# Kernel optimization log

Hardware: AMD Instinct MI355X
Metric: run time of the kernel (lower is better)

Reference implementation:

```python
import math
import jax, jax.numpy as jnp
import numpy as np

BS, N, D, H = 4, 512, 1024, 16
HD = D // H


def setup_inputs() -> dict:
    key = jax.random.key(0)
    ks = jax.random.split(key, 12)
    s = 1.0 / math.sqrt(D)
    return {
        "x": jax.random.normal(ks[0], (BS, N, D), jnp.float32),
        "r": jax.random.normal(ks[1], (BS, 3, N, N), jnp.float32),
        "bias": jax.random.normal(ks[2], (BS, H, N, N), jnp.float32),
        "mask": jax.random.randint(ks[3], (BS, 1, N, N), 0, 2, jnp.int32),
        "wq": jax.random.normal(ks[4], (D, D), jnp.float32) * s,
        "bq": jnp.zeros((D,), jnp.float32),
        "wk": jax.random.normal(ks[5], (D, D), jnp.float32) * s,
        "bk": jnp.zeros((D,), jnp.float32),
        "wv": jax.random.normal(ks[6], (D, D), jnp.float32) * s,
        "bv": jnp.zeros((D,), jnp.float32),
        "wo": jax.random.normal(ks[7], (D, 1), jnp.float32) * s,
        "bo": jnp.zeros((1,), jnp.float32),
    }


def reference(x, r, bias, mask, wq, bq, wk, bk, wv, bv, wo, bo):
    bs, n, d = x.shape
    # projections -> (bs, h, n, hd)
    q = (x @ wq + bq).reshape(bs, n, H, HD).transpose(0, 2, 1, 3)
    k = (x @ wk + bk).reshape(bs, n, H, HD).transpose(0, 2, 1, 3)
    v = (x @ wv + bv).reshape(bs, n, H, HD).transpose(0, 2, 1, 3)
    logits = jnp.einsum("bhid,bhjd->bhij", q, k) / math.sqrt(HD) + bias
    logits = jnp.where(mask == 0, jnp.float32(-1e9), logits)
    w = jax.nn.softmax(logits, axis=-1)  # (bs,h,n,n)
    # o[b,i,c,h,d] = sum_j r[b,c,i,j] * w[b,h,i,j] * v[b,h,j,d]
    o = jnp.einsum("bcij,bhij,bhjd->bichd", r, w, v)
    o = o.reshape(bs, n, 3, d)
    force = o @ wo + bo  # (bs, n, 3, 1)
    return force
```

## Files before the change

kernel.cpp:

```cpp
#include <hip/hip_runtime.h>
#include <stdint.h>

#define BSZ 4
#define NSEQ 512
#define DMOD 1024
#define NH 16
#define HD 64

typedef __attribute__((ext_vector_type(8))) short bf16x8;
typedef __attribute__((ext_vector_type(4))) float f32x4;

__device__ __forceinline__ unsigned short f2bf(float f) {
    union { float f; uint32_t u; } v; v.f = f;
    uint32_t u = v.u;
    u += 0x7FFFu + ((u >> 16) & 1u);
    return (unsigned short)(u >> 16);
}

__device__ __forceinline__ void gload_lds16(const unsigned short* g, unsigned short* l) {
    __builtin_amdgcn_global_load_lds(
        (const __attribute__((address_space(1))) void*)g,
        (__attribute__((address_space(3))) void*)l, 16, 0, 0);
}

__global__ __launch_bounds__(256) void k_prep(
        const float* __restrict__ x, const float* __restrict__ wq, const float* __restrict__ wk,
        const float* __restrict__ wv, const float* __restrict__ bv, const float* __restrict__ wo,
        unsigned short* __restrict__ xb, unsigned short* __restrict__ wqt,
        unsigned short* __restrict__ wkt, float* __restrict__ wv2t, float* __restrict__ bv2) {
    __shared__ float t[32][33];
    int bx = blockIdx.x, tid = threadIdx.x;
    if (bx < 2048) {
        int i = bx * 256 + tid;
        float4 v = ((const float4*)x)[i];
        ushort4 o; o.x = f2bf(v.x); o.y = f2bf(v.y); o.z = f2bf(v.z); o.w = f2bf(v.w);
        ((ushort4*)xb)[i] = o;
    } else if (bx < 4096) {
        int g = bx - 2048; int z = g >> 10; g &= 1023;
        const float* src = z ? wk : wq;
        unsigned short* dst = z ? wkt : wqt;
        int be = (g & 31) * 32, bc = (g >> 5) * 32;
        int tx = tid & 31, ty = tid >> 5;
        #pragma unroll
        for (int yy = 0; yy < 32; yy += 8)
            t[ty + yy][tx] = src[(size_t)(be + ty + yy) * DMOD + bc + tx];
        __syncthreads();
        #pragma unroll
        for (int yy = 0; yy < 32; yy += 8)
            dst[(size_t)(bc + ty + yy) * DMOD + be + tx] = f2bf(t[tx][ty + yy]);
    } else {
        int g = bx - 4096;
        int grp = tid >> 6, l = tid & 63;
        int e = g * 4 + grp;
        float out = 0.f;
        #pragma unroll
        for (int it = 0; it < 16; ++it) {
            float v = wv[(size_t)e * DMOD + it * 64 + l] * wo[it * 64 + l];
            #pragma unroll
            for (int off = 1; off < 64; off <<= 1) v += __shfl_xor(v, off, 64);
            if (l == it) out = v;
        }
        if (l < 16) wv2t[l * DMOD + e] = out;
        if (g == 0 && grp == 0) {
            float ob = 0.f;
            #pragma unroll
            for (int it = 0; it < 16; ++it) {
                float v = bv[it * 64 + l] * wo[it * 64 + l];
                #pragma unroll
                for (int off = 1; off < 64; off <<= 1) v += __shfl_xor(v, off, 64);
                if (l == it) ob = v;
            }
            if (l < 16) bv2[l] = ob;
        }
    }
}

__global__ __launch_bounds__(256) void k_mid(
        const float* __restrict__ x, const float* __restrict__ wv2t, const float* __restrict__ bv2,
        const unsigned short* __restrict__ xb, const unsigned short* __restrict__ wqt,
        const unsigned short* __restrict__ wkt, const float* __restrict__ bq,
        const float* __restrict__ bk, float* __restrict__ u,
        unsigned short* __restrict__ qT, unsigned short* __restrict__ kT) {
    __shared__ unsigned short lA[64 * 128];
    __shared__ unsigned short lB[64 * 128];
    int bx = blockIdx.x, tid = threadIdx.x;
    if (bx < 512) {
        int wave = bx * 4 + (tid >> 6);
        int l = tid & 63;
        int b = wave >> 9, j = wave & 511;
        const float* xr = x + (size_t)(b * NSEQ + j) * DMOD;
        float p[16];
        #pragma unroll
        for (int h = 0; h < 16; ++h) p[h] = 0.f;
        for (int it = 0; it < 16; ++it) {
            int e = l + it * 64;
            float xv = xr[e];
            #pragma unroll
            for (int h = 0; h < 16; ++h) p[h] += xv * wv2t[h * DMOD + e];
        }
        #pragma unroll
        for (int h = 0; h < 16; ++h) {
            #pragma unroll
            for (int off = 1; off < 64; off <<= 1) p[h] += __shfl_xor(p[h], off, 64);
        }
        float out = 0.f;
        #pragma unroll
        for (int h = 0; h < 16; ++h) if (l == h) out = p[h] + bv2[h];
        if (l < 16) u[(b * 16 + l) * NSEQ + j] = out;
        return;
    }
    int g = bx - 512;
    int z = g >> 9;
    const unsigned short* Wt = z ? wkt : wqt;
    const float* bias = z ? bk : bq;
    unsigned short* outT = z ? kT : qT;
    float scale = z ? 1.f : 0.125f;
    int w = tid >> 6, lane = tid & 63;
    int quad = lane >> 4, col = lane & 15;
    int m0 = (g & 31) * 64;
    int n0 = ((g >> 5) & 15) * 64;

    f32x4 acc[4];
    #pragma unroll
    for (int nt = 0; nt < 4; ++nt) acc[nt] = (f32x4){0.f, 0.f, 0.f, 0.f};

    int rl_base = lane >> 4;
    int cs = lane & 15;
    int asw = cs & 7;

    for (int kc = 0; kc < 8; ++kc) {
        int k0 = kc * 128;
        #pragma unroll
        for (int t = 0; t < 4; ++t) {
            int rl = t * 4 + rl_base;
            int row = w * 16 + rl;
            int cg = cs ^ (rl & 7);
            gload_lds16(xb + (size_t)(m0 + row) * DMOD + k0 + cg * 8,
                        &lA[(w * 16 + t * 4) * 128]);
            gload_lds16(Wt + (size_t)(n0 + row) * DMOD + k0 + cg * 8,
                        &lB[(w * 16 + t * 4) * 128]);
        }
        __syncthreads();
        int arow = w * 16 + cs;
        #pragma unroll
        for (int ks = 0; ks < 4; ++ks) {
            int blk = (ks * 4 + quad) ^ asw;
            bf16x8 af = *(const bf16x8*)&lA[arow * 128 + blk * 8];
            #pragma unroll
            for (int nt = 0; nt < 4; ++nt) {
                bf16x8 bfr = *(const bf16x8*)&lB[(nt * 16 + cs) * 128 + blk * 8];
                acc[nt] = __builtin_amdgcn_mfma_f32_16x16x32_bf16(af, bfr, acc[nt], 0, 0, 0);
            }
        }
        __syncthreads();
    }
    #pragma unroll
    for (int nt = 0; nt < 4; ++nt) {
        int n = n0 + nt * 16 + col;
        int h = n >> 6, d = n & 63;
        float bvv = bias[n];
        #pragma unroll
        for (int r = 0; r < 4; ++r) {
            int mg = m0 + w * 16 + quad * 4 + r;
            int b = mg >> 9, i = mg & 511;
            outT[(size_t)((b * 16 + h) * NSEQ + i) * HD + d] = f2bf((acc[nt][r] + bvv) * scale);
        }
    }
}

#define RSTRIDE 68
__global__ __launch_bounds__(512) void k_attn(
        const unsigned short* __restrict__ qT, const unsigned short* __restrict__ kT,
        const float* __restrict__ bias, const int* __restrict__ mask,
        const float* __restrict__ u, const float* __restrict__ r,
        float* __restrict__ spart, float* __restrict__ P) {
    __shared__ float rT[3 * 16 * RSTRIDE];
    int tid = threadIdx.x;
    int w = tid >> 6, lane = tid & 63;
    int quad = lane >> 4, col = lane & 15;
    int it = blockIdx.x, jc = blockIdx.y, b = blockIdx.z;
    int i0 = it * 16, j0 = jc * 64;

    #pragma unroll
    for (int t = 0; t < 6; ++t) {
        int idx = t * 512 + tid;
        int c = idx >> 10, rem = idx & 1023;
        int i = rem >> 6, j = rem & 63;
        rT[(c * 16 + i) * RSTRIDE + j] =
            r[((size_t)(b * 3 + c) * NSEQ + i0 + i) * NSEQ + j0 + j];
    }
    const int* mrow = mask + (size_t)b * NSEQ * NSEQ;
    __syncthreads();

    #pragma unroll
    for (int hrep = 0; hrep < 2; ++hrep) {
        int h = w + hrep * 8;
        int bh = b * 16 + h;
        const unsigned short* qbase = qT + ((size_t)(bh * NSEQ + i0 + col)) * HD + quad * 8;
        bf16x8 a0 = *(const bf16x8*)qbase;
        bf16x8 a1 = *(const bf16x8*)(qbase + 32);
        const float* brow = bias + (size_t)bh * NSEQ * NSEQ;
        const float* ub = u + (size_t)bh * NSEQ;
        float sp[4] = {0.f, 0.f, 0.f, 0.f};
        float pc0[4] = {0.f, 0.f, 0.f, 0.f};
        float pc1[4] = {0.f, 0.f, 0.f, 0.f};
        float pc2[4] = {0.f, 0.f, 0.f, 0.f};
        #pragma unroll
        for (int jt = 0; jt < 4; ++jt) {
            int jb = j0 + jt * 16;
            const unsigned short* kbase = kT + ((size_t)(bh * NSEQ + jb + col)) * HD + quad * 8;
            bf16x8 b0 = *(const bf16x8*)kbase;
            bf16x8 b1 = *(const bf16x8*)(kbase + 32);
            f32x4 acc = (f32x4){0.f, 0.f, 0.f, 0.f};
            acc = __builtin_amdgcn_mfma_f32_16x16x32_bf16(a0, b0, acc, 0, 0, 0);
            acc = __builtin_amdgcn_mfma_f32_16x16x32_bf16(a1, b1, acc, 0, 0, 0);
            int j = jb + col;
            float uv = ub[j];
            int jl = jt * 16 + col;
            #pragma unroll
            for (int rr = 0; rr < 4; ++rr) {
                int i = i0 + quad * 4 + rr;
                float lg = acc[rr] + brow[(size_t)i * NSEQ + j];
                int mk = mrow[(size_t)i * NSEQ + j];
                float e = (mk == 0) ? 0.f : __expf(lg);
                sp[rr] += e;
                float eu = e * uv;
                int il = quad * 4 + rr;
                pc0[rr] += eu * rT[(0 * 16 + il) * RSTRIDE + jl];
                pc1[rr] += eu * rT[(1 * 16 + il) * RSTRIDE + jl];
                pc2[rr] += eu * rT[(2 * 16 + il) * RSTRIDE + jl];
            }
        }
        #pragma unroll
        for (int rr = 0; rr < 4; ++rr) {
            #pragma unroll
            for (int off = 1; off < 16; off <<= 1) {
                sp[rr]  += __shfl_xor(sp[rr], off, 64);
                pc0[rr] += __shfl_xor(pc0[rr], off, 64);
                pc1[rr] += __shfl_xor(pc1[rr], off, 64);
                pc2[rr] += __shfl_xor(pc2[rr], off, 64);
            }
        }
        if (col == 0) {
            #pragma unroll
            for (int rr = 0; rr < 4; ++rr) {
                int il = quad * 4 + rr;
                spart[((size_t)bh * NSEQ + i0 + il) * 8 + jc] = sp[rr];
                size_t pb = ((((size_t)(b * 16 + h) * 32 + it) * 8 + jc) * 16 + il) * 3;
                P[pb + 0] = pc0[rr];
                P[pb + 1] = pc1[rr];
                P[pb + 2] = pc2[rr];
            }
        }
    }
}

__global__ __launch_bounds__(256) void k_final(
        const float* __restrict__ spart, const float* __restrict__ P,
        const float* __restrict__ bo, float* __restrict__ out) {
    int tid = threadIdx.x;
    int rloc = tid >> 4, h = tid & 15;
    int row = blockIdx.x * 16 + rloc;
    int b = row >> 9, i = row & 511;
    int it = i >> 4, il = i & 15;
    int bh = b * 16 + h;
    const float* sprow = spart + ((size_t)bh * NSEQ + i) * 8;
    float4 sa = *(const float4*)sprow;
    float4 sb = *(const float4*)(sprow + 4);
    float s = sa.x + sa.y + sa.z + sa.w + sb.x + sb.y + sb.z + sb.w;
    float sinv = (s > 0.f) ? 1.f / s : 0.f;
    float f0 = 0.f, f1 = 0.f, f2 = 0.f;
    #pragma unroll
    for (int jc = 0; jc < 8; ++jc) {
        size_t pb = ((((size_t)(b * 16 + h) * 32 + it) * 8 + jc) * 16 + il) * 3;
        f0 += P[pb]; f1 += P[pb + 1]; f2 += P[pb + 2];
    }
    f0 *= sinv; f1 *= sinv; f2 *= sinv;
    #pragma unroll
    for (int off = 1; off < 16; off <<= 1) {
        f0 += __shfl_xor(f0, off, 64);
        f1 += __shfl_xor(f1, off, 64);
        f2 += __shfl_xor(f2, off, 64);
    }
    if (h == 0) {
        float bov = bo[0];
        out[(size_t)row * 3 + 0] = f0 + bov;
        out[(size_t)row * 3 + 1] = f1 + bov;
        out[(size_t)row * 3 + 2] = f2 + bov;
    }
}

extern "C" void kernel_launch(void* const* d_in, const int* in_sizes, int n_in,
                              void* d_out, int out_size, void* d_ws, size_t ws_size,
                              hipStream_t stream) {
    const float* x    = (const float*)d_in[0];
    const float* rr   = (const float*)d_in[1];
    const float* bias = (const float*)d_in[2];
    const int*   mask = (const int*)d_in[3];
    const float* wq   = (const float*)d_in[4];
    const float* bq   = (const float*)d_in[5];
    const float* wk   = (const float*)d_in[6];
    const float* bk   = (const float*)d_in[7];
    const float* wv   = (const float*)d_in[8];
    const float* bv   = (const float*)d_in[9];
    const float* wo   = (const float*)d_in[10];
    const float* bo   = (const float*)d_in[11];
    float* out = (float*)d_out;

    char* ws = (char*)d_ws;
    unsigned short* xb    = (unsigned short*)(ws + 0);
    unsigned short* wqt   = (unsigned short*)(ws + 4194304);
    unsigned short* wkt   = (unsigned short*)(ws + 6291456);
    float*          wv2t  = (float*)(ws + 8388608);
    float*          bv2   = (float*)(ws + 8454144);
    float*          u     = (float*)(ws + 8454400);
    unsigned short* qT    = (unsigned short*)(ws + 8585472);
    unsigned short* kT    = (unsigned short*)(ws + 12779776);
    float*          spart = (float*)(ws + 16974080);
    float*          P     = (float*)(ws + 18022656);

    k_prep<<<4352, 256, 0, stream>>>(x, wq, wk, wv, bv, wo, xb, wqt, wkt, wv2t, bv2);
    k_mid<<<1536, 256, 0, stream>>>(x, wv2t, bv2, xb, wqt, wkt, bq, bk, u, qT, kT);
    k_attn<<<dim3(32, 8, 4), 512, 0, stream>>>(qT, kT, bias, mask, u, rr, spart, P);
    k_final<<<128, 256, 0, stream>>>(spart, P, bo, out);
}
```

Measured before the change: 223.0 us.

## Split attention heads across two blocks and prefetch bias/mask/K before sync

The attention kernel now launches twice as many blocks, each handling 8 heads instead of 16, with launch_bounds requesting 2 blocks per CU. All per-thread global loads for Q, K fragments, bias, mask and u are issued before the barrier so they overlap with the shared-memory fill of r. This targets memory latency and low occupancy in the bias-streaming phase. The cost is that r tiles are loaded twice (once per head group) and register pressure rises from the prefetched arrays.

```diff
diff --git a/kernel.cpp b/kernel.cpp
--- a/kernel.cpp
+++ b/kernel.cpp
@@ -169,7 +169,7 @@
 }
 
 #define RSTRIDE 68
-__global__ __launch_bounds__(512) void k_attn(
+__global__ __launch_bounds__(512, 2) void k_attn(
         const unsigned short* __restrict__ qT, const unsigned short* __restrict__ kT,
         const float* __restrict__ bias, const int* __restrict__ mask,
         const float* __restrict__ u, const float* __restrict__ r,
@@ -178,8 +178,11 @@
     int tid = threadIdx.x;
     int w = tid >> 6, lane = tid & 63;
     int quad = lane >> 4, col = lane & 15;
-    int it = blockIdx.x, jc = blockIdx.y, b = blockIdx.z;
+    int it = blockIdx.x, jc = blockIdx.y, bz = blockIdx.z;
+    int b = bz >> 1, hg = bz & 1;
     int i0 = it * 16, j0 = jc * 64;
+    int h = hg * 8 + w;
+    int bh = b * 16 + h;
 
     #pragma unroll
     for (int t = 0; t < 6; ++t) {
@@ -189,68 +192,81 @@
         rT[(c * 16 + i) * RSTRIDE + j] =
             r[((size_t)(b * 3 + c) * NSEQ + i0 + i) * NSEQ + j0 + j];
     }
+
+    const unsigned short* qbase = qT + ((size_t)(bh * NSEQ + i0 + col)) * HD + quad * 8;
+    bf16x8 a0 = *(const bf16x8*)qbase;
+    bf16x8 a1 = *(const bf16x8*)(qbase + 32);
+
+    bf16x8 kf0[4], kf1[4];
+    #pragma unroll
+    for (int jt = 0; jt < 4; ++jt) {
+        const unsigned short* kbase = kT + ((size_t)(bh * NSEQ + j0 + jt * 16 + col)) * HD + quad * 8;
+        kf0[jt] = *(const bf16x8*)kbase;
+        kf1[jt] = *(const bf16x8*)(kbase + 32);
+    }
+    const float* brow = bias + (size_t)bh * NSEQ * NSEQ;
     const int* mrow = mask + (size_t)b * NSEQ * NSEQ;
+    float bvv[16];
+    int mkv[16];
+    #pragma unroll
+    for (int jt = 0; jt < 4; ++jt) {
+        int j = j0 + jt * 16 + col;
+        #pragma unroll
+        for (int rr = 0; rr < 4; ++rr) {
+            int i = i0 + quad * 4 + rr;
+            bvv[jt * 4 + rr] = brow[(size_t)i * NSEQ + j];
+            mkv[jt * 4 + rr] = mrow[(size_t)i * NSEQ + j];
+        }
+    }
+    const float* ub = u + (size_t)bh * NSEQ;
+    float uvv[4];
+    #pragma unroll
+    for (int jt = 0; jt < 4; ++jt) uvv[jt] = ub[j0 + jt * 16 + col];
+
     __syncthreads();
 
-    #pragma unroll
-    for (int hrep = 0; hrep < 2; ++hrep) {
-        int h = w + hrep * 8;
-        int bh = b * 16 + h;
-        const unsigned short* qbase = qT + ((size_t)(bh * NSEQ + i0 + col)) * HD + quad * 8;
-        bf16x8 a0 = *(const bf16x8*)qbase;
-        bf16x8 a1 = *(const bf16x8*)(qbase + 32);
-        const float* brow = bias + (size_t)bh * NSEQ * NSEQ;
-        const float* ub = u + (size_t)bh * NSEQ;
-        float sp[4] = {0.f, 0.f, 0.f, 0.f};
-        float pc0[4] = {0.f, 0.f, 0.f, 0.f};
-        float pc1[4] = {0.f, 0.f, 0.f, 0.f};
-        float pc2[4] = {0.f, 0.f, 0.f, 0.f};
-        #pragma unroll
-        for (int jt = 0; jt < 4; ++jt) {
-            int jb = j0 + jt * 16;
-            const unsigned short* kbase = kT + ((size_t)(bh * NSEQ + jb + col)) * HD + quad * 8;
-            bf16x8 b0 = *(const bf16x8*)kbase;
-            bf16x8 b1 = *(const bf16x8*)(kbase + 32);
-            f32x4 acc = (f32x4){0.f, 0.f, 0.f, 0.f};
-            acc = __builtin_amdgcn_mfma_f32_16x16x32_bf16(a0, b0, acc, 0, 0, 0);
-            acc = __builtin_amdgcn_mfma_f32_16x16x32_bf16(a1, b1, acc, 0, 0, 0);
-            int j = jb + col;
-            float uv = ub[j];
-            int jl = jt * 16 + col;
-            #pragma unroll
-            for (int rr = 0; rr < 4; ++rr) {
-                int i = i0 + quad * 4 + rr;
-                float lg = acc[rr] + brow[(size_t)i * NSEQ + j];
-                int mk = mrow[(size_t)i * NSEQ + j];
-                float e = (mk == 0) ? 0.f : __expf(lg);
-                sp[rr] += e;
-                float eu = e * uv;
-                int il = quad * 4 + rr;
-                pc0[rr] += eu * rT[(0 * 16 + il) * RSTRIDE + jl];
-                pc1[rr] += eu * rT[(1 * 16 + il) * RSTRIDE + jl];
-                pc2[rr] += eu * rT[(2 * 16 + il) * RSTRIDE + jl];
-            }
-        }
+    float sp[4] = {0.f, 0.f, 0.f, 0.f};
+    float pc0[4] = {0.f, 0.f, 0.f, 0.f};
+    float pc1[4] = {0.f, 0.f, 0.f, 0.f};
+    float pc2[4] = {0.f, 0.f, 0.f, 0.f};
+    #pragma unroll
+    for (int jt = 0; jt < 4; ++jt) {
+        f32x4 acc = (f32x4){0.f, 0.f, 0.f, 0.f};
+        acc = __builtin_amdgcn_mfma_f32_16x16x32_bf16(a0, kf0[jt], acc, 0, 0, 0);
+        acc = __builtin_amdgcn_mfma_f32_16x16x32_bf16(a1, kf1[jt], acc, 0, 0, 0);
+        float uv = uvv[jt];
+        int jl = jt * 16 + col;
         #pragma unroll
         for (int rr = 0; rr < 4; ++rr) {
-            #pragma unroll
-            for (int off = 1; off < 16; off <<= 1) {
-                sp[rr]  += __shfl_xor(sp[rr], off, 64);
-                pc0[rr] += __shfl_xor(pc0[rr], off, 64);
-                pc1[rr] += __shfl_xor(pc1[rr], off, 64);
-                pc2[rr] += __shfl_xor(pc2[rr], off, 64);
-            }
-        }
-        if (col == 0) {
-            #pragma unroll
-            for (int rr = 0; rr < 4; ++rr) {
-                int il = quad * 4 + rr;
-                spart[((size_t)bh * NSEQ + i0 + il) * 8 + jc] = sp[rr];
-                size_t pb = ((((size_t)(b * 16 + h) * 32 + it) * 8 + jc) * 16 + il) * 3;
-                P[pb + 0] = pc0[rr];
-                P[pb + 1] = pc1[rr];
-                P[pb + 2] = pc2[rr];
-            }
+            float lg = acc[rr] + bvv[jt * 4 + rr];
+            float e = (mkv[jt * 4 + rr] == 0) ? 0.f : __expf(lg);
+            sp[rr] += e;
+            float eu = e * uv;
+            int il = quad * 4 + rr;
+            pc0[rr] += eu * rT[(0 * 16 + il) * RSTRIDE + jl];
+            pc1[rr] += eu * rT[(1 * 16 + il) * RSTRIDE + jl];
+            pc2[rr] += eu * rT[(2 * 16 + il) * RSTRIDE + jl];
+        }
+    }
+    #pragma unroll
+    for (int rr = 0; rr < 4; ++rr) {
+        #pragma unroll
+        for (int off = 1; off < 16; off <<= 1) {
+            sp[rr]  += __shfl_xor(sp[rr], off, 64);
+            pc0[rr] += __shfl_xor(pc0[rr], off, 64);
+            pc1[rr] += __shfl_xor(pc1[rr], off, 64);
+            pc2[rr] += __shfl_xor(pc2[rr], off, 64);
+        }
+    }
+    if (col == 0) {
+        #pragma unroll
+        for (int rr = 0; rr < 4; ++rr) {
+            int il = quad * 4 + rr;
+            spart[((size_t)bh * NSEQ + i0 + il) * 8 + jc] = sp[rr];
+            size_t pb = ((((size_t)(b * 16 + h) * 32 + it) * 8 + jc) * 16 + il) * 3;
+            P[pb + 0] = pc0[rr];
+            P[pb + 1] = pc1[rr];
+            P[pb + 2] = pc2[rr];
         }
     }
 }
@@ -321,6 +337,6 @@
 
     k_prep<<<4352, 256, 0, stream>>>(x, wq, wk, wv, bv, wo, xb, wqt, wkt, wv2t, bv2);
     k_mid<<<1536, 256, 0, stream>>>(x, wv2t, bv2, xb, wqt, wkt, bq, bk, u, qT, kT);
-    k_attn<<<dim3(32, 8, 4), 512, 0, stream>>>(qT, kT, bias, mask, u, rr, spart, P);
+    k_attn<<<dim3(32, 8, 8), 512, 0, stream>>>(qT, kT, bias, mask, u, rr, spart, P);
     k_final<<<128, 256, 0, stream>>>(spart, P, bo, out);
 }
```

Result: faster. 191.3 us (-14.2%).
